# Kernel tuning notes

Measured on AMD Instinct MI355X. Metric: run time of the kernel, lower is better.

The kernel has to match this reference:

```python
import jax, jax.numpy as jnp
import numpy as np

B, T, C = 2, 2048, 1024
H = 16
HS = C // H
EPS = 1e-5


def layernorm(x, g, b):
    mu = jnp.mean(x, axis=-1, keepdims=True)
    var = jnp.var(x, axis=-1, keepdims=True)
    return (x - mu) * jax.lax.rsqrt(var + EPS) * g + b


def setup_inputs() -> dict:
    key = jax.random.key(0)
    ks = jax.random.split(key, 12)
    s_in = 1.0 / np.sqrt(C)
    s_ff = 1.0 / np.sqrt(4 * C)
    return {
        "x": jax.random.normal(ks[0], (B, T, C), jnp.float32),
        "Wq": jax.random.normal(ks[1], (H, C, HS), jnp.float32) * s_in,
        "Wk": jax.random.normal(ks[2], (H, C, HS), jnp.float32) * s_in,
        "Wv": jax.random.normal(ks[3], (H, C, HS), jnp.float32) * s_in,
        "Wo": jax.random.normal(ks[4], (C, C), jnp.float32) * s_in,
        "bo": jnp.zeros((C,), jnp.float32),
        "W1": jax.random.normal(ks[5], (C, 4 * C), jnp.float32) * s_in,
        "b1": jnp.zeros((4 * C,), jnp.float32),
        "W2": jax.random.normal(ks[6], (4 * C, C), jnp.float32) * s_ff,
        "b2": jnp.zeros((C,), jnp.float32),
        "g1": jnp.ones((C,), jnp.float32),
        "be1": jnp.zeros((C,), jnp.float32),
        "g2": jnp.ones((C,), jnp.float32),
        "be2": jnp.zeros((C,), jnp.float32),
    }


def reference(x, Wq, Wk, Wv, Wo, bo, W1, b1, W2, b2, g1, be1, g2, be2):
    # x: [B,T,C]. Dropout is identity (eval mode).
    x = layernorm(x, g1, be1)
    # --- multi-head causal self-attention (per-source: scale by C**-0.5, NOT head_size) ---
    q = jnp.einsum("btc,hcd->bhtd", x, Wq)
    k = jnp.einsum("btc,hcd->bhtd", x, Wk)
    v = jnp.einsum("btc,hcd->bhtd", x, Wv)
    scores = jnp.einsum("bhtd,bhsd->bhts", q, k) * (C ** -0.5)  # [B,H,T,T]
    causal = jnp.tril(jnp.ones((T, T), bool))
    scores = jnp.where(causal, scores, -jnp.inf)
    wei = jax.nn.softmax(scores, axis=-1)
    attn = jnp.einsum("bhts,bhsd->bhtd", wei, v)
    attn = attn.transpose(0, 2, 1, 3).reshape(B, T, C)  # concat heads on last dim
    sa = attn @ Wo + bo
    x = x + sa
    # --- MLP with second pre-op LayerNorm ---
    x = layernorm(x, g2, be2)
    h = jax.nn.relu(x @ W1 + b1)
    x = x + (h @ W2 + b2)
    return x
```

## Files before the change

### kernel.cpp

```cpp
#include <hip/hip_runtime.h>
#include <hip/hip_bf16.h>
#include <math.h>

#define B_ 2
#define T_ 2048
#define C_ 1024
#define H_ 16
#define HS_ 64
#define N_ROWS (B_*T_)
#define MB (1024*1024)

typedef __attribute__((ext_vector_type(8))) short bf16x8;
typedef __attribute__((ext_vector_type(8))) unsigned short u16x8;
typedef __attribute__((ext_vector_type(4))) float floatx4;

static __device__ __forceinline__ unsigned short f2bf(float f) {
  union { float f; unsigned u; } v; v.f = f;
  unsigned r = v.u + 0x7fff + ((v.u >> 16) & 1);
  return (unsigned short)(r >> 16);
}
static __device__ __forceinline__ float bf2f(unsigned short s) {
  union { unsigned u; float f; } v; v.u = ((unsigned)s) << 16;
  return v.f;
}

__global__ __launch_bounds__(256) void ln_kernel(
    const float* __restrict__ x, const float* __restrict__ g,
    const float* __restrict__ b, unsigned short* __restrict__ outb)
{
  const int row = blockIdx.x;
  const int tid = threadIdx.x;
  const float* xr = x + (size_t)row * C_;
  float4 xv = *reinterpret_cast<const float4*>(xr + tid * 4);
  float s  = xv.x + xv.y + xv.z + xv.w;
  float ss = xv.x*xv.x + xv.y*xv.y + xv.z*xv.z + xv.w*xv.w;
  #pragma unroll
  for (int off = 32; off > 0; off >>= 1) {
    s  += __shfl_down(s, off, 64);
    ss += __shfl_down(ss, off, 64);
  }
  __shared__ float rs[4], rss[4];
  __shared__ float smu, srstd;
  if ((tid & 63) == 0) { rs[tid >> 6] = s; rss[tid >> 6] = ss; }
  __syncthreads();
  if (tid == 0) {
    float S  = rs[0] + rs[1] + rs[2] + rs[3];
    float SS = rss[0] + rss[1] + rss[2] + rss[3];
    float mu  = S * (1.0f / C_);
    float var = SS * (1.0f / C_) - mu * mu;
    smu = mu; srstd = rsqrtf(var + 1e-5f);
  }
  __syncthreads();
  const float mu = smu, rstd = srstd;
  float4 gv = *reinterpret_cast<const float4*>(g + tid * 4);
  float4 bv = *reinterpret_cast<const float4*>(b + tid * 4);
  union { unsigned long long ll; unsigned short s[4]; } o;
  o.s[0] = f2bf((xv.x - mu) * rstd * gv.x + bv.x);
  o.s[1] = f2bf((xv.y - mu) * rstd * gv.y + bv.y);
  o.s[2] = f2bf((xv.z - mu) * rstd * gv.z + bv.z);
  o.s[3] = f2bf((xv.w - mu) * rstd * gv.w + bv.w);
  *reinterpret_cast<unsigned long long*>(outb + (size_t)row * C_ + tid * 4) = o.ll;
}

__global__ __launch_bounds__(256) void transpose_cast(
    const float* __restrict__ in, unsigned short* __restrict__ out, int R, int Cc)
{
  __shared__ float tile[32][33];
  const int bz = blockIdx.z;
  in  += (size_t)bz * R * Cc;
  out += (size_t)bz * R * Cc;
  const int tx = threadIdx.x & 31;
  const int ty = threadIdx.x >> 5;
  const int c0 = blockIdx.x * 32, r0 = blockIdx.y * 32;
  #pragma unroll
  for (int j = 0; j < 4; ++j)
    tile[ty + j*8][tx] = in[(size_t)(r0 + ty + j*8) * Cc + c0 + tx];
  __syncthreads();
  #pragma unroll
  for (int j = 0; j < 4; ++j)
    out[(size_t)(c0 + ty + j*8) * R + r0 + tx] = f2bf(tile[tx][ty + j*8]);
}

__global__ __launch_bounds__(256) void transpose_cast_qkv(
    const float* __restrict__ Wq, const float* __restrict__ Wk,
    const float* __restrict__ Wv, unsigned short* __restrict__ out)
{
  __shared__ float tile[32][33];
  const int z = blockIdx.z;
  const int which = z >> 4, h = z & 15;
  const float* in = (which == 0 ? Wq : which == 1 ? Wk : Wv) + (size_t)h * C_ * HS_;
  unsigned short* dst = out + (size_t)z * C_ * HS_;
  const int tx = threadIdx.x & 31;
  const int ty = threadIdx.x >> 5;
  const int c0 = blockIdx.x * 32, r0 = blockIdx.y * 32;
  #pragma unroll
  for (int j = 0; j < 4; ++j)
    tile[ty + j*8][tx] = in[(size_t)(r0 + ty + j*8) * HS_ + c0 + tx];
  __syncthreads();
  #pragma unroll
  for (int j = 0; j < 4; ++j)
    dst[(size_t)(c0 + ty + j*8) * C_ + r0 + tx] = f2bf(tile[tx][ty + j*8]);
}

template<int TNB, bool OUTBF16, bool RELU, bool HASB, bool HASRES>
__global__ __launch_bounds__(256) void gemm_bf16(
    const unsigned short* __restrict__ A,
    const unsigned short* __restrict__ Bt,
    const float* __restrict__ bias,
    const unsigned short* __restrict__ res,
    void* __restrict__ Cout,
    int M, int N, int K)
{
  constexpr int NT = TNB / 32;
  constexpr int WN = TNB / 2;
  __shared__ unsigned short As[2][128 * 32];
  __shared__ unsigned short Bs[2][TNB * 32];
  const int tid  = threadIdx.x;
  const int lane = tid & 63;
  const int wave = tid >> 6;
  const int wm = wave & 1, wn = wave >> 1;
  const int m0 = blockIdx.x * 128, n0 = blockIdx.y * TNB;

  const int lrow = lane >> 2;
  const int lcol = (lane & 3) * 8;
  const int fr = lane & 15;
  const int fq = lane >> 4;

  floatx4 acc[4][NT] = {};

  const unsigned short* Aw = A  + (size_t)m0 * K;
  const unsigned short* Bw = Bt + (size_t)n0 * K;

  for (int k0 = 0; k0 < K; k0 += 64) {
    __syncthreads();
    #pragma unroll
    for (int half = 0; half < 2; ++half) {
      #pragma unroll
      for (int i = 0; i < 2; ++i) {
        const int rbase = i * 64 + wave * 16;
        const unsigned short* gp =
            Aw + (size_t)(rbase + lrow) * K + k0 + half * 32 + lcol;
        __builtin_amdgcn_global_load_lds(
            (const __attribute__((address_space(1))) void*)gp,
            (__attribute__((address_space(3))) void*)(As[half] + rbase * 32),
            16, 0, 0);
      }
      #pragma unroll
      for (int i = 0; i < TNB / 64; ++i) {
        const int rbase = i * 64 + wave * 16;
        const unsigned short* gp =
            Bw + (size_t)(rbase + lrow) * K + k0 + half * 32 + lcol;
        __builtin_amdgcn_global_load_lds(
            (const __attribute__((address_space(1))) void*)gp,
            (__attribute__((address_space(3))) void*)(Bs[half] + rbase * 32),
            16, 0, 0);
      }
    }
    __syncthreads();

    #pragma unroll
    for (int half = 0; half < 2; ++half) {
      bf16x8 af[4], bfr[NT];
      #pragma unroll
      for (int t = 0; t < 4; ++t)
        af[t]  = *reinterpret_cast<const bf16x8*>(
            As[half] + (wm*64 + t*16 + fr)*32 + fq*8);
      #pragma unroll
      for (int t = 0; t < NT; ++t)
        bfr[t] = *reinterpret_cast<const bf16x8*>(
            Bs[half] + (wn*WN + t*16 + fr)*32 + fq*8);
      #pragma unroll
      for (int mt = 0; mt < 4; ++mt)
        #pragma unroll
        for (int nt = 0; nt < NT; ++nt)
          acc[mt][nt] = __builtin_amdgcn_mfma_f32_16x16x32_bf16(
              af[mt], bfr[nt], acc[mt][nt], 0, 0, 0);
    }
  }

  #pragma unroll
  for (int nt = 0; nt < NT; ++nt) {
    const int col = n0 + wn*WN + nt*16 + fr;
    const float bv = HASB ? bias[col] : 0.0f;
    #pragma unroll
    for (int mt = 0; mt < 4; ++mt) {
      #pragma unroll
      for (int r = 0; r < 4; ++r) {
        const int row = m0 + wm*64 + mt*16 + fq*4 + r;
        float v = acc[mt][nt][r] + bv;
        if (RELU) v = v > 0.0f ? v : 0.0f;
        if (HASRES) v += bf2f(res[(size_t)row * N + col]);
        if (OUTBF16) ((unsigned short*)Cout)[(size_t)row * N + col] = f2bf(v);
        else         ((float*)Cout)[(size_t)row * N + col] = v;
      }
    }
  }
}

template<int TNB, int SPLITS>
__global__ __launch_bounds__(256) void gemm_splitk(
    const unsigned short* __restrict__ A,
    const unsigned short* __restrict__ Bt,
    unsigned short* __restrict__ Cpart,
    int M, int N, int Kfull)
{
  constexpr int NT = TNB / 32;
  constexpr int WN = TNB / 2;
  __shared__ unsigned short As[2][128 * 32];
  __shared__ unsigned short Bs[2][TNB * 32];
  const int tid  = threadIdx.x;
  const int lane = tid & 63;
  const int wave = tid >> 6;
  const int wm = wave & 1, wn = wave >> 1;
  const int m0 = blockIdx.x * 128, n0 = blockIdx.y * TNB;
  const int z  = blockIdx.z;
  const int Kh = Kfull / SPLITS;

  const int lrow = lane >> 2;
  const int lcol = (lane & 3) * 8;
  const int fr = lane & 15;
  const int fq = lane >> 4;

  floatx4 acc[4][NT] = {};

  const unsigned short* Aw = A  + (size_t)m0 * Kfull + (size_t)z * Kh;
  const unsigned short* Bw = Bt + (size_t)n0 * Kfull + (size_t)z * Kh;
  unsigned short* Cw = Cpart + (size_t)z * M * N;

  for (int k0 = 0; k0 < Kh; k0 += 64) {
    __syncthreads();
    #pragma unroll
    for (int half = 0; half < 2; ++half) {
      #pragma unroll
      for (int i = 0; i < 2; ++i) {
        const int rbase = i * 64 + wave * 16;
        const unsigned short* gp =
            Aw + (size_t)(rbase + lrow) * Kfull + k0 + half * 32 + lcol;
        __builtin_amdgcn_global_load_lds(
            (const __attribute__((address_space(1))) void*)gp,
            (__attribute__((address_space(3))) void*)(As[half] + rbase * 32),
            16, 0, 0);
      }
      #pragma unroll
      for (int i = 0; i < TNB / 64; ++i) {
        const int rbase = i * 64 + wave * 16;
        const unsigned short* gp =
            Bw + (size_t)(rbase + lrow) * Kfull + k0 + half * 32 + lcol;
        __builtin_amdgcn_global_load_lds(
            (const __attribute__((address_space(1))) void*)gp,
            (__attribute__((address_space(3))) void*)(Bs[half] + rbase * 32),
            16, 0, 0);
      }
    }
    __syncthreads();

    #pragma unroll
    for (int half = 0; half < 2; ++half) {
      bf16x8 af[4], bfr[NT];
      #pragma unroll
      for (int t = 0; t < 4; ++t)
        af[t]  = *reinterpret_cast<const bf16x8*>(
            As[half] + (wm*64 + t*16 + fr)*32 + fq*8);
      #pragma unroll
      for (int t = 0; t < NT; ++t)
        bfr[t] = *reinterpret_cast<const bf16x8*>(
            Bs[half] + (wn*WN + t*16 + fr)*32 + fq*8);
      #pragma unroll
      for (int mt = 0; mt < 4; ++mt)
        #pragma unroll
        for (int nt = 0; nt < NT; ++nt)
          acc[mt][nt] = __builtin_amdgcn_mfma_f32_16x16x32_bf16(
              af[mt], bfr[nt], acc[mt][nt], 0, 0, 0);
    }
  }

  #pragma unroll
  for (int nt = 0; nt < NT; ++nt) {
    const int col = n0 + wn*WN + nt*16 + fr;
    #pragma unroll
    for (int mt = 0; mt < 4; ++mt)
      #pragma unroll
      for (int r = 0; r < 4; ++r) {
        const int row = m0 + wm*64 + mt*16 + fq*4 + r;
        Cw[(size_t)row * N + col] = f2bf(acc[mt][nt][r]);
      }
  }
}

template<int SPLITS>
__global__ __launch_bounds__(256) void splitk_reduce(
    const unsigned short* __restrict__ p,
    const float* __restrict__ bias, const unsigned short* __restrict__ res,
    float* __restrict__ out)
{
  const size_t i = ((size_t)blockIdx.x * 256 + threadIdx.x) * 4;
  const size_t MN = (size_t)N_ROWS * C_;
  float4 bv = *reinterpret_cast<const float4*>(bias + (i & (size_t)(C_ - 1)));
  float acc[4] = {bv.x, bv.y, bv.z, bv.w};
  {
    const unsigned short* rp = res + i;
    #pragma unroll
    for (int j = 0; j < 4; ++j) acc[j] += bf2f(rp[j]);
  }
  #pragma unroll
  for (int z = 0; z < SPLITS; ++z) {
    const unsigned short* pp = p + (size_t)z * MN + i;
    #pragma unroll
    for (int j = 0; j < 4; ++j) acc[j] += bf2f(pp[j]);
  }
  float4 o; o.x = acc[0]; o.y = acc[1]; o.z = acc[2]; o.w = acc[3];
  *reinterpret_cast<float4*>(out + i) = o;
}

__global__ __launch_bounds__(256) void v_transpose(
    const unsigned short* __restrict__ qkv, unsigned short* __restrict__ vt)
{
  __shared__ __align__(16) unsigned short sT[64][72];
  const int st = blockIdx.x;
  const int bh = blockIdx.y;
  const int b = bh >> 4, h = bh & 15;
  const int t = threadIdx.x;
  const int r = t >> 2, c0 = (t & 3) * 16;
  const unsigned short* src =
      qkv + (size_t)(b * T_ + st * 64 + r) * 3072 + 2048 + h * 64 + c0;
  *(u16x8*)&sT[r][c0]     = *(const u16x8*)src;
  *(u16x8*)&sT[r][c0 + 8] = *(const u16x8*)(src + 8);
  __syncthreads();
  const int d = t >> 2, sc = (t & 3) * 16;
  unsigned short v[16];
  #pragma unroll
  for (int j = 0; j < 16; ++j) v[j] = sT[sc + j][d];
  unsigned short* dst = vt + ((size_t)bh * 64 + d) * (size_t)T_ + st * 64 + sc;
  *(uint4*)dst       = *(uint4*)&v[0];
  *(uint4*)(dst + 8) = *(uint4*)&v[8];
}

__global__ __launch_bounds__(256, 4) void attn_mfma(
    const unsigned short* __restrict__ qkv,
    const unsigned short* __restrict__ vt,
    unsigned short* __restrict__ out)
{
  const int bh = blockIdx.x;
  const int b = bh >> 4, h = bh & 15;
  const int tid = threadIdx.x;
  const int w = tid >> 6;
  const int lane = tid & 63;
  const int l15 = lane & 15, fq = lane >> 4;

  __shared__ __align__(16) unsigned short sK [128][72];
  __shared__ __align__(16) unsigned short sVt[64][136];
  __shared__ __align__(16) unsigned short sP [64][136];

  const float c1 = 1.4426950408889634f / 32.0f;

  #pragma unroll 1
  for (int pass = 0; pass < 2; ++pass) {
    const int qt = pass ? 31 - (int)blockIdx.y : (int)blockIdx.y;
    const int t0 = qt * 64;
    const int q_row = t0 + w * 16 + l15;

    bf16x8 aq[2];
    {
      const unsigned short* qp = qkv + (size_t)(b*T_ + q_row)*3072 + h*HS_ + fq*8;
      aq[0] = *(const bf16x8*)qp;
      aq[1] = *(const bf16x8*)(qp + 32);
    }

    floatx4 oacc[4] = {};
    float m_s = -3.0e38f, l_s = 0.0f;
    const int nks = (qt >> 1) + 1;

    #pragma unroll 1
    for (int ks = 0; ks < nks; ++ks) {
      __syncthreads();
      {
        const int r  = tid >> 1, c0 = (tid & 1) * 32;
        const unsigned short* kp =
            qkv + (size_t)(b*T_ + ks*128 + r)*3072 + C_ + h*HS_ + c0;
        u16x8 k0 = *(const u16x8*)kp;
        u16x8 k1 = *(const u16x8*)(kp + 8);
        u16x8 k2 = *(const u16x8*)(kp + 16);
        u16x8 k3 = *(const u16x8*)(kp + 24);
        const int r2 = tid >> 2, c2 = (tid & 3) * 32;
        const unsigned short* vp =
            vt + ((size_t)bh*64 + r2)*(size_t)T_ + ks*128 + c2;
        u16x8 v0 = *(const u16x8*)vp;
        u16x8 v1 = *(const u16x8*)(vp + 8);
        u16x8 v2 = *(const u16x8*)(vp + 16);
        u16x8 v3 = *(const u16x8*)(vp + 24);
        *(u16x8*)&sK[r][c0]        = k0; *(u16x8*)&sK[r][c0 + 8]   = k1;
        *(u16x8*)&sK[r][c0 + 16]   = k2; *(u16x8*)&sK[r][c0 + 24]  = k3;
        *(u16x8*)&sVt[r2][c2]      = v0; *(u16x8*)&sVt[r2][c2 + 8] = v1;
        *(u16x8*)&sVt[r2][c2 + 16] = v2; *(u16x8*)&sVt[r2][c2 + 24] = v3;
      }
      __syncthreads();

      floatx4 stacc[8] = {};
      __builtin_amdgcn_s_setprio(1);
      #pragma unroll
      for (int st = 0; st < 8; ++st) {
        bf16x8 k0 = *(const bf16x8*)&sK[st*16 + l15][fq*8];
        bf16x8 k1 = *(const bf16x8*)&sK[st*16 + l15][32 + fq*8];
        stacc[st] = __builtin_amdgcn_mfma_f32_16x16x32_bf16(k0, aq[0], stacc[st], 0, 0, 0);
        stacc[st] = __builtin_amdgcn_mfma_f32_16x16x32_bf16(k1, aq[1], stacc[st], 0, 0, 0);
      }
      __builtin_amdgcn_s_setprio(0);

      if (ks == nks - 1) {
        const int sbase = ks*128 + fq*4;
        #pragma unroll
        for (int st = 0; st < 8; ++st)
          #pragma unroll
          for (int r = 0; r < 4; ++r)
            if (sbase + st*16 + r > q_row) stacc[st][r] = -3.0e38f;
      }

      float mx = -3.0e38f;
      #pragma unroll
      for (int st = 0; st < 8; ++st)
        #pragma unroll
        for (int r = 0; r < 4; ++r) mx = fmaxf(mx, stacc[st][r]);
      mx = fmaxf(mx, __shfl_xor(mx, 16, 64));
      mx = fmaxf(mx, __shfl_xor(mx, 32, 64));

      float mnew;
      if (__all((mx - m_s) * c1 <= 8.0f)) {
        mnew = m_s;
      } else {
        mnew = fmaxf(m_s, mx);
        const float alpha = exp2f((m_s - mnew) * c1);
        #pragma unroll
        for (int r = 0; r < 4; ++r) {
          const float ar = __shfl(alpha, fq*4 + r, 64);
          #pragma unroll
          for (int dt = 0; dt < 4; ++dt) oacc[dt][r] *= ar;
        }
        l_s *= alpha;
        m_s = mnew;
      }

      const float mc = mnew * c1;
      float sum = 0.0f;
      #pragma unroll
      for (int st = 0; st < 8; ++st) {
        unsigned pu[4];
        #pragma unroll
        for (int r = 0; r < 4; ++r) {
          const float p = exp2f(stacc[st][r] * c1 - mc);
          sum += p;
          union { float f; unsigned u; } cv; cv.f = p;
          pu[r] = cv.u + 0x8000u;
        }
        const unsigned lo = __builtin_amdgcn_perm(pu[1], pu[0], 0x07060302u);
        const unsigned hi = __builtin_amdgcn_perm(pu[3], pu[2], 0x07060302u);
        *(unsigned long long*)&sP[w*16 + l15][st*16 + fq*4] =
            ((unsigned long long)hi << 32) | lo;
      }
      sum += __shfl_xor(sum, 16, 64);
      sum += __shfl_xor(sum, 32, 64);
      l_s += sum;

      __builtin_amdgcn_s_setprio(1);
      #pragma unroll
      for (int c = 0; c < 4; ++c) {
        bf16x8 ap = *(const bf16x8*)&sP[w*16 + l15][c*32 + fq*8];
        #pragma unroll
        for (int dt = 0; dt < 4; ++dt) {
          bf16x8 bv = *(const bf16x8*)&sVt[dt*16 + l15][c*32 + fq*8];
          oacc[dt] = __builtin_amdgcn_mfma_f32_16x16x32_bf16(ap, bv, oacc[dt], 0, 0, 0);
        }
      }
      __builtin_amdgcn_s_setprio(0);
    }

    #pragma unroll
    for (int r = 0; r < 4; ++r) {
      const float il = 1.0f / __shfl(l_s, fq*4 + r, 64);
      const int q = t0 + w*16 + fq*4 + r;
      #pragma unroll
      for (int dt = 0; dt < 4; ++dt)
        out[(size_t)(b*T_ + q)*C_ + h*HS_ + dt*16 + l15] = f2bf(oacc[dt][r] * il);
    }
  }
}

extern "C" void kernel_launch(void* const* d_in, const int* in_sizes, int n_in,
                              void* d_out, int out_size, void* d_ws, size_t ws_size,
                              hipStream_t stream)
{
  const float* x   = (const float*)d_in[0];
  const float* Wq  = (const float*)d_in[1];
  const float* Wk  = (const float*)d_in[2];
  const float* Wv  = (const float*)d_in[3];
  const float* Wo  = (const float*)d_in[4];
  const float* bo  = (const float*)d_in[5];
  const float* W1  = (const float*)d_in[6];
  const float* b1  = (const float*)d_in[7];
  const float* W2  = (const float*)d_in[8];
  const float* b2  = (const float*)d_in[9];
  const float* g1  = (const float*)d_in[10];
  const float* be1 = (const float*)d_in[11];
  const float* g2  = (const float*)d_in[12];
  const float* be2 = (const float*)d_in[13];
  float* out = (float*)d_out;

  char* ws = (char*)d_ws;
  unsigned short* BtQKV = (unsigned short*)(ws + (size_t) 0*MB);
  unsigned short* BtWo  = (unsigned short*)(ws + (size_t) 6*MB);
  unsigned short* BtW1  = (unsigned short*)(ws + (size_t) 8*MB);
  unsigned short* BtW2  = (unsigned short*)(ws + (size_t)16*MB);
  unsigned short* lnb   = (unsigned short*)(ws + (size_t)24*MB);
  unsigned short* qkvb  = (unsigned short*)(ws + (size_t)32*MB);
  unsigned short* vtb   = (unsigned short*)(ws + (size_t)56*MB);
  unsigned short* attnb = (unsigned short*)(ws + (size_t)64*MB);
  float*          x2    = (float*)         (ws + (size_t)32*MB);
  unsigned short* hb    = (unsigned short*)(ws + (size_t)32*MB);
  unsigned short* pk4   = (unsigned short*)(ws + (size_t)64*MB);

  dim3 blk(256);

  transpose_cast_qkv<<<dim3(HS_/32, C_/32, 3*H_), blk, 0, stream>>>(Wq, Wk, Wv, BtQKV);
  transpose_cast<<<dim3(C_/32,  C_/32, 1),  blk, 0, stream>>>(Wo, BtWo, C_, C_);
  transpose_cast<<<dim3(4*C_/32,C_/32, 1),  blk, 0, stream>>>(W1, BtW1, C_, 4*C_);
  transpose_cast<<<dim3(C_/32,4*C_/32, 1),  blk, 0, stream>>>(W2, BtW2, 4*C_, C_);

  ln_kernel<<<dim3(N_ROWS), blk, 0, stream>>>(x, g1, be1, lnb);

  gemm_bf16<128,true,false,false,false><<<dim3(N_ROWS/128, 3072/128), blk, 0, stream>>>(
      lnb, BtQKV, nullptr, nullptr, qkvb, N_ROWS, 3072, C_);

  v_transpose<<<dim3(T_/64, B_*H_), blk, 0, stream>>>(qkvb, vtb);

  attn_mfma<<<dim3(B_*H_, T_/128), blk, 0, stream>>>(qkvb, vtb, attnb);

  gemm_bf16<64,false,false,true,true><<<dim3(N_ROWS/128, C_/64), blk, 0, stream>>>(
      attnb, BtWo, bo, lnb, x2, N_ROWS, C_, C_);

  ln_kernel<<<dim3(N_ROWS), blk, 0, stream>>>(x2, g2, be2, lnb);

  gemm_bf16<128,true,true,true,false><<<dim3(N_ROWS/128, 4*C_/128), blk, 0, stream>>>(
      lnb, BtW1, b1, nullptr, hb, N_ROWS, 4*C_, C_);

  gemm_splitk<128,4><<<dim3(N_ROWS/128, C_/128, 4), blk, 0, stream>>>(
      hb, BtW2, pk4, N_ROWS, C_, 4*C_);

  splitk_reduce<4><<<dim3((N_ROWS * C_) / (256 * 4)), blk, 0, stream>>>(
      pk4, b2, lnb, out);
}
```

Before: 358.1 us.

## Prefetch next K/V tile into registers and launch one query tile per block

The attention kernel no longer pairs a short and a long query tile inside one block over two passes. It now launches one 64-row query tile per block, ordered heaviest-first, and doubles the grid. Inside the key loop, the global loads for the next K/V tile are issued into registers before the current tile's MFMA and softmax work, and are stored to shared memory after a barrier, so load latency overlaps compute. It also switches to the hardware exp2 builtin and lowers the launch-bounds occupancy hint from 4 to 3 to leave room for the extra prefetch registers.

```diff
diff --git a/kernel.cpp b/kernel.cpp
--- a/kernel.cpp
+++ b/kernel.cpp
@@ -335,17 +335,20 @@
   *(uint4*)(dst + 8) = *(uint4*)&v[8];
 }
 
-__global__ __launch_bounds__(256, 4) void attn_mfma(
+__global__ __launch_bounds__(256, 3) void attn_mfma(
     const unsigned short* __restrict__ qkv,
     const unsigned short* __restrict__ vt,
     unsigned short* __restrict__ out)
 {
   const int bh = blockIdx.x;
+  const int qt = (int)(gridDim.y - 1) - (int)blockIdx.y;
   const int b = bh >> 4, h = bh & 15;
   const int tid = threadIdx.x;
   const int w = tid >> 6;
   const int lane = tid & 63;
   const int l15 = lane & 15, fq = lane >> 4;
+  const int t0 = qt * 64;
+  const int q_row = t0 + w * 16 + l15;
 
   __shared__ __align__(16) unsigned short sK [128][72];
   __shared__ __align__(16) unsigned short sVt[64][136];
@@ -353,134 +356,143 @@
 
   const float c1 = 1.4426950408889634f / 32.0f;
 
+  bf16x8 aq[2];
+  {
+    const unsigned short* qp = qkv + (size_t)(b*T_ + q_row)*3072 + h*HS_ + fq*8;
+    aq[0] = *(const bf16x8*)qp;
+    aq[1] = *(const bf16x8*)(qp + 32);
+  }
+
+  const int nks = (qt >> 1) + 1;
+
+  const int kr = tid >> 1, kc = (tid & 1) * 32;
+  const int vr = tid >> 2, vc = (tid & 3) * 32;
+  const unsigned short* kp0 =
+      qkv + (size_t)(b*T_ + kr)*3072 + C_ + h*HS_ + kc;
+  const unsigned short* vp0 =
+      vt + ((size_t)bh*64 + vr)*(size_t)T_ + vc;
+
+  u16x8 kg0, kg1, kg2, kg3, vg0, vg1, vg2, vg3;
+  kg0 = *(const u16x8*)kp0;      kg1 = *(const u16x8*)(kp0 + 8);
+  kg2 = *(const u16x8*)(kp0+16); kg3 = *(const u16x8*)(kp0 + 24);
+  vg0 = *(const u16x8*)vp0;      vg1 = *(const u16x8*)(vp0 + 8);
+  vg2 = *(const u16x8*)(vp0+16); vg3 = *(const u16x8*)(vp0 + 24);
+  *(u16x8*)&sK [kr][kc]      = kg0; *(u16x8*)&sK [kr][kc + 8]  = kg1;
+  *(u16x8*)&sK [kr][kc + 16] = kg2; *(u16x8*)&sK [kr][kc + 24] = kg3;
+  *(u16x8*)&sVt[vr][vc]      = vg0; *(u16x8*)&sVt[vr][vc + 8]  = vg1;
+  *(u16x8*)&sVt[vr][vc + 16] = vg2; *(u16x8*)&sVt[vr][vc + 24] = vg3;
+
+  floatx4 oacc[4] = {};
+  float m_s = -3.0e38f, l_s = 0.0f;
+
   #pragma unroll 1
-  for (int pass = 0; pass < 2; ++pass) {
-    const int qt = pass ? 31 - (int)blockIdx.y : (int)blockIdx.y;
-    const int t0 = qt * 64;
-    const int q_row = t0 + w * 16 + l15;
-
-    bf16x8 aq[2];
-    {
-      const unsigned short* qp = qkv + (size_t)(b*T_ + q_row)*3072 + h*HS_ + fq*8;
-      aq[0] = *(const bf16x8*)qp;
-      aq[1] = *(const bf16x8*)(qp + 32);
-    }
-
-    floatx4 oacc[4] = {};
-    float m_s = -3.0e38f, l_s = 0.0f;
-    const int nks = (qt >> 1) + 1;
-
-    #pragma unroll 1
-    for (int ks = 0; ks < nks; ++ks) {
-      __syncthreads();
-      {
-        const int r  = tid >> 1, c0 = (tid & 1) * 32;
-        const unsigned short* kp =
-            qkv + (size_t)(b*T_ + ks*128 + r)*3072 + C_ + h*HS_ + c0;
-        u16x8 k0 = *(const u16x8*)kp;
-        u16x8 k1 = *(const u16x8*)(kp + 8);
-        u16x8 k2 = *(const u16x8*)(kp + 16);
-        u16x8 k3 = *(const u16x8*)(kp + 24);
-        const int r2 = tid >> 2, c2 = (tid & 3) * 32;
-        const unsigned short* vp =
-            vt + ((size_t)bh*64 + r2)*(size_t)T_ + ks*128 + c2;
-        u16x8 v0 = *(const u16x8*)vp;
-        u16x8 v1 = *(const u16x8*)(vp + 8);
-        u16x8 v2 = *(const u16x8*)(vp + 16);
-        u16x8 v3 = *(const u16x8*)(vp + 24);
-        *(u16x8*)&sK[r][c0]        = k0; *(u16x8*)&sK[r][c0 + 8]   = k1;
-        *(u16x8*)&sK[r][c0 + 16]   = k2; *(u16x8*)&sK[r][c0 + 24]  = k3;
-        *(u16x8*)&sVt[r2][c2]      = v0; *(u16x8*)&sVt[r2][c2 + 8] = v1;
-        *(u16x8*)&sVt[r2][c2 + 16] = v2; *(u16x8*)&sVt[r2][c2 + 24] = v3;
-      }
-      __syncthreads();
-
-      floatx4 stacc[8] = {};
-      __builtin_amdgcn_s_setprio(1);
-      #pragma unroll
-      for (int st = 0; st < 8; ++st) {
-        bf16x8 k0 = *(const bf16x8*)&sK[st*16 + l15][fq*8];
-        bf16x8 k1 = *(const bf16x8*)&sK[st*16 + l15][32 + fq*8];
-        stacc[st] = __builtin_amdgcn_mfma_f32_16x16x32_bf16(k0, aq[0], stacc[st], 0, 0, 0);
-        stacc[st] = __builtin_amdgcn_mfma_f32_16x16x32_bf16(k1, aq[1], stacc[st], 0, 0, 0);
-      }
-      __builtin_amdgcn_s_setprio(0);
-
-      if (ks == nks - 1) {
-        const int sbase = ks*128 + fq*4;
-        #pragma unroll
-        for (int st = 0; st < 8; ++st)
-          #pragma unroll
-          for (int r = 0; r < 4; ++r)
-            if (sbase + st*16 + r > q_row) stacc[st][r] = -3.0e38f;
-      }
-
-      float mx = -3.0e38f;
+  for (int ks = 0; ks < nks; ++ks) {
+    asm volatile("s_waitcnt lgkmcnt(0)" ::: "memory");
+    __builtin_amdgcn_s_barrier();
+
+    if (ks + 1 < nks) {
+      const unsigned short* kp = kp0 + (size_t)(ks + 1) * (128 * 3072);
+      kg0 = *(const u16x8*)kp;        kg1 = *(const u16x8*)(kp + 8);
+      kg2 = *(const u16x8*)(kp + 16); kg3 = *(const u16x8*)(kp + 24);
+      const unsigned short* vp = vp0 + (ks + 1) * 128;
+      vg0 = *(const u16x8*)vp;        vg1 = *(const u16x8*)(vp + 8);
+      vg2 = *(const u16x8*)(vp + 16); vg3 = *(const u16x8*)(vp + 24);
+    }
+
+    floatx4 stacc[8] = {};
+    __builtin_amdgcn_s_setprio(1);
+    #pragma unroll
+    for (int st = 0; st < 8; ++st) {
+      bf16x8 ka = *(const bf16x8*)&sK[st*16 + l15][fq*8];
+      bf16x8 kb = *(const bf16x8*)&sK[st*16 + l15][32 + fq*8];
+      stacc[st] = __builtin_amdgcn_mfma_f32_16x16x32_bf16(ka, aq[0], stacc[st], 0, 0, 0);
+      stacc[st] = __builtin_amdgcn_mfma_f32_16x16x32_bf16(kb, aq[1], stacc[st], 0, 0, 0);
+    }
+    __builtin_amdgcn_s_setprio(0);
+
+    if (ks == nks - 1) {
+      const int sbase = ks*128 + fq*4;
       #pragma unroll
       for (int st = 0; st < 8; ++st)
         #pragma unroll
-        for (int r = 0; r < 4; ++r) mx = fmaxf(mx, stacc[st][r]);
-      mx = fmaxf(mx, __shfl_xor(mx, 16, 64));
-      mx = fmaxf(mx, __shfl_xor(mx, 32, 64));
-
-      float mnew;
-      if (__all((mx - m_s) * c1 <= 8.0f)) {
-        mnew = m_s;
-      } else {
-        mnew = fmaxf(m_s, mx);
-        const float alpha = exp2f((m_s - mnew) * c1);
+        for (int r = 0; r < 4; ++r)
+          if (sbase + st*16 + r > q_row) stacc[st][r] = -3.0e38f;
+    }
+
+    float mx = -3.0e38f;
+    #pragma unroll
+    for (int st = 0; st < 8; ++st)
+      #pragma unroll
+      for (int r = 0; r < 4; ++r) mx = fmaxf(mx, stacc[st][r]);
+    mx = fmaxf(mx, __shfl_xor(mx, 16, 64));
+    mx = fmaxf(mx, __shfl_xor(mx, 32, 64));
+
+    float mnew;
+    if (__all((mx - m_s) * c1 <= 8.0f)) {
+      mnew = m_s;
+    } else {
+      mnew = fmaxf(m_s, mx);
+      const float alpha = __builtin_amdgcn_exp2f((m_s - mnew) * c1);
+      #pragma unroll
+      for (int r = 0; r < 4; ++r) {
+        const float ar = __shfl(alpha, fq*4 + r, 64);
         #pragma unroll
-        for (int r = 0; r < 4; ++r) {
-          const float ar = __shfl(alpha, fq*4 + r, 64);
-          #pragma unroll
-          for (int dt = 0; dt < 4; ++dt) oacc[dt][r] *= ar;
-        }
-        l_s *= alpha;
-        m_s = mnew;
-      }
-
-      const float mc = mnew * c1;
-      float sum = 0.0f;
-      #pragma unroll
-      for (int st = 0; st < 8; ++st) {
-        unsigned pu[4];
-        #pragma unroll
-        for (int r = 0; r < 4; ++r) {
-          const float p = exp2f(stacc[st][r] * c1 - mc);
-          sum += p;
-          union { float f; unsigned u; } cv; cv.f = p;
-          pu[r] = cv.u + 0x8000u;
-        }
-        const unsigned lo = __builtin_amdgcn_perm(pu[1], pu[0], 0x07060302u);
-        const unsigned hi = __builtin_amdgcn_perm(pu[3], pu[2], 0x07060302u);
-        *(unsigned long long*)&sP[w*16 + l15][st*16 + fq*4] =
-            ((unsigned long long)hi << 32) | lo;
-      }
-      sum += __shfl_xor(sum, 16, 64);
-      sum += __shfl_xor(sum, 32, 64);
-      l_s += sum;
-
-      __builtin_amdgcn_s_setprio(1);
-      #pragma unroll
-      for (int c = 0; c < 4; ++c) {
-        bf16x8 ap = *(const bf16x8*)&sP[w*16 + l15][c*32 + fq*8];
-        #pragma unroll
-        for (int dt = 0; dt < 4; ++dt) {
-          bf16x8 bv = *(const bf16x8*)&sVt[dt*16 + l15][c*32 + fq*8];
-          oacc[dt] = __builtin_amdgcn_mfma_f32_16x16x32_bf16(ap, bv, oacc[dt], 0, 0, 0);
-        }
-      }
-      __builtin_amdgcn_s_setprio(0);
-    }
-
-    #pragma unroll
-    for (int r = 0; r < 4; ++r) {
-      const float il = 1.0f / __shfl(l_s, fq*4 + r, 64);
-      const int q = t0 + w*16 + fq*4 + r;
-      #pragma unroll
-      for (int dt = 0; dt < 4; ++dt)
-        out[(size_t)(b*T_ + q)*C_ + h*HS_ + dt*16 + l15] = f2bf(oacc[dt][r] * il);
-    }
+        for (int dt = 0; dt < 4; ++dt) oacc[dt][r] *= ar;
+      }
+      l_s *= alpha;
+      m_s = mnew;
+    }
+
+    const float mc = mnew * c1;
+    float sum = 0.0f;
+    #pragma unroll
+    for (int st = 0; st < 8; ++st) {
+      unsigned pu[4];
+      #pragma unroll
+      for (int r = 0; r < 4; ++r) {
+        const float p = __builtin_amdgcn_exp2f(stacc[st][r] * c1 - mc);
+        sum += p;
+        union { float f; unsigned u; } cv; cv.f = p;
+        pu[r] = cv.u + 0x8000u;
+      }
+      const unsigned lo = __builtin_amdgcn_perm(pu[1], pu[0], 0x07060302u);
+      const unsigned hi = __builtin_amdgcn_perm(pu[3], pu[2], 0x07060302u);
+      *(unsigned long long*)&sP[w*16 + l15][st*16 + fq*4] =
+          ((unsigned long long)hi << 32) | lo;
+    }
+    sum += __shfl_xor(sum, 16, 64);
+    sum += __shfl_xor(sum, 32, 64);
+    l_s += sum;
+
+    __builtin_amdgcn_s_setprio(1);
+    #pragma unroll
+    for (int c = 0; c < 4; ++c) {
+      bf16x8 ap = *(const bf16x8*)&sP[w*16 + l15][c*32 + fq*8];
+      #pragma unroll
+      for (int dt = 0; dt < 4; ++dt) {
+        bf16x8 bv = *(const bf16x8*)&sVt[dt*16 + l15][c*32 + fq*8];
+        oacc[dt] = __builtin_amdgcn_mfma_f32_16x16x32_bf16(ap, bv, oacc[dt], 0, 0, 0);
+      }
+    }
+    __builtin_amdgcn_s_setprio(0);
+
+    asm volatile("s_waitcnt lgkmcnt(0)" ::: "memory");
+    __builtin_amdgcn_s_barrier();
+    if (ks + 1 < nks) {
+      *(u16x8*)&sK [kr][kc]      = kg0; *(u16x8*)&sK [kr][kc + 8]  = kg1;
+      *(u16x8*)&sK [kr][kc + 16] = kg2; *(u16x8*)&sK [kr][kc + 24] = kg3;
+      *(u16x8*)&sVt[vr][vc]      = vg0; *(u16x8*)&sVt[vr][vc + 8]  = vg1;
+      *(u16x8*)&sVt[vr][vc + 16] = vg2; *(u16x8*)&sVt[vr][vc + 24] = vg3;
+    }
+  }
+
+  #pragma unroll
+  for (int r = 0; r < 4; ++r) {
+    const float il = 1.0f / __shfl(l_s, fq*4 + r, 64);
+    const int q = t0 + w*16 + fq*4 + r;
+    #pragma unroll
+    for (int dt = 0; dt < 4; ++dt)
+      out[(size_t)(b*T_ + q)*C_ + h*HS_ + dt*16 + l15] = f2bf(oacc[dt][r] * il);
   }
 }
 
@@ -531,7 +543,7 @@
 
   v_transpose<<<dim3(T_/64, B_*H_), blk, 0, stream>>>(qkvb, vtb);
 
-  attn_mfma<<<dim3(B_*H_, T_/128), blk, 0, stream>>>(qkvb, vtb, attnb);
+  attn_mfma<<<dim3(B_*H_, T_/64), blk, 0, stream>>>(qkvb, vtb, attnb);
 
   gemm_bf16<64,false,false,true,true><<<dim3(N_ROWS/128, C_/64), blk, 0, stream>>>(
       attnb, BtWo, bo, lnb, x2, N_ROWS, C_, C_);
```

Measured after the change: 355.9 us. About the same (-0.6%).
